# Performance work log

Measured on AMD Instinct MI355X. Metric: run time of the kernel, lower is better.

The kernel has to match this reference:

```python
import jax, jax.numpy as jnp
import numpy as np

D_MODEL = 1024
N_HEADS = 16
HEAD_DIM = D_MODEL // N_HEADS  # 64
BASE = 10000.0
MAX_X, MAX_Y, MAX_Z = 32, 32, 8
NEG_INF = -1e9  # stand-in for float('-inf') in masked_fill; identical after softmax


def _split_dims(head_dim):
    n_pairs = head_dim // 2
    px = n_pairs // 3
    py = n_pairs // 3
    pz = n_pairs - px - py
    return px * 2, py * 2, pz * 2


def _cos_sin_table(dim, max_pos):
    # matches RotaryEmbedding3D._register_cache
    inv_freq = 1.0 / (BASE ** (np.arange(0, dim, 2, dtype=np.float32) / dim))
    t = np.arange(max_pos, dtype=np.float32)[:, None] * inv_freq  # [max_pos, dim/2]
    cos = np.repeat(np.cos(t), 2, axis=-1)  # repeat_interleave(2)
    sin = np.repeat(np.sin(t), 2, axis=-1)
    return jnp.asarray(cos), jnp.asarray(sin)


def _rotate_half(x):
    x1 = x[..., ::2]
    x2 = x[..., 1::2]
    return jnp.stack((-x2, x1), axis=-1).reshape(x.shape)


def setup_inputs() -> dict:
    key = jax.random.key(0)
    k1, k2, k3, k4, k5, k6 = jax.random.split(key, 6)
    B, S = 2, 2048
    hidden_states = jax.random.normal(k1, (B, S, D_MODEL), dtype=jnp.float32)
    w_qkv = jax.random.normal(k2, (D_MODEL, 3 * D_MODEL), dtype=jnp.float32) * 0.02
    w_out = jax.random.normal(k3, (D_MODEL, D_MODEL), dtype=jnp.float32) * 0.02
    px = jax.random.randint(k4, (B, S, 1), 0, MAX_X)
    py = jax.random.randint(k5, (B, S, 1), 0, MAX_Y)
    pz = jax.random.randint(k6, (B, S, 1), 0, MAX_Z)
    pos_xyz = jnp.concatenate([px, py, pz], axis=-1).astype(jnp.int64)
    causal_mask = jnp.triu(jnp.ones((S, S), dtype=bool), k=1)[None, None]  # [1,1,S,S]
    return {"hidden_states": hidden_states, "w_qkv": w_qkv, "w_out": w_out,
            "pos_xyz": pos_xyz, "causal_mask": causal_mask}


def reference(hidden_states, w_qkv, w_out, pos_xyz, causal_mask):
    B, S, D = hidden_states.shape
    H, Hd = N_HEADS, HEAD_DIM
    # fused QKV projection
    qkv = hidden_states @ w_qkv  # [B,S,3D]
    qkv = qkv.reshape(B, S, 3, H, Hd).transpose(2, 0, 3, 1, 4)  # [3,B,H,S,Hd]
    q, k, v = qkv[0], qkv[1], qkv[2]
    # 3D RoPE tables and lookups
    dx, dy, dz = _split_dims(Hd)
    cx, sx = _cos_sin_table(dx, MAX_X)
    cy, sy = _cos_sin_table(dy, MAX_Y)
    cz, sz = _cos_sin_table(dz, MAX_Z)
    ix = jnp.clip(pos_xyz[..., 0], 0, MAX_X - 1)
    iy = jnp.clip(pos_xyz[..., 1], 0, MAX_Y - 1)
    iz = jnp.clip(pos_xyz[..., 2], 0, MAX_Z - 1)
    cos = jnp.concatenate([cx[ix], cy[iy], cz[iz]], axis=-1)[:, None]  # [B,1,S,Hd]
    sin = jnp.concatenate([sx[ix], sy[iy], sz[iz]], axis=-1)[:, None]
    q = q * cos + _rotate_half(q) * sin
    k = k * cos + _rotate_half(k) * sin
    # SDPA with causal bias
    scale = Hd ** -0.5
    scores = jnp.einsum('bhqd,bhkd->bhqk', q, k) * scale
    scores = jnp.where(causal_mask, jnp.asarray(NEG_INF, scores.dtype), scores)
    probs = jax.nn.softmax(scores, axis=-1)
    attn = jnp.einsum('bhqk,bhkd->bhqd', probs, v)
    attn = attn.transpose(0, 2, 1, 3).reshape(B, S, D)
    return attn @ w_out
```

## Files before the change

### kernel.cpp

```cpp
#include <hip/hip_runtime.h>
#include <hip/hip_bf16.h>
#include <math.h>

typedef __bf16 bf16;
typedef __bf16 bf16x8 __attribute__((ext_vector_type(8)));
typedef float f32x4 __attribute__((ext_vector_type(4)));

#define SEQ 2048
#define NHEADS 16
#define HDIM 64
#define DM 1024
#define QKVW 3072
#define NEGBIG -1.0e30f

__device__ __forceinline__ void gload_lds16(const void* g, void* l) {
  __builtin_amdgcn_global_load_lds(
      (const __attribute__((address_space(1))) unsigned int*)g,
      (__attribute__((address_space(3))) unsigned int*)l, 16, 0, 0);
}

template <int CTRL>
__device__ __forceinline__ float dppmovf(float x) {
  return __builtin_bit_cast(
      float, __builtin_amdgcn_mov_dpp(__builtin_bit_cast(int, x), CTRL, 0xf,
                                      0xf, true));
}
__device__ __forceinline__ float rowsum16(float x) {
  x += dppmovf<0xB1>(x);
  x += dppmovf<0x4E>(x);
  x += dppmovf<0x124>(x);
  x += dppmovf<0x128>(x);
  return x;
}

__global__ __launch_bounds__(256) void cvt_f32_bf16(
    const float* __restrict__ in, bf16* __restrict__ out) {
  int i = (blockIdx.x * 256 + threadIdx.x) * 8;
  float4 a = *(const float4*)(in + i);
  float4 b = *(const float4*)(in + i + 4);
  bf16x8 o;
  o[0] = (bf16)a.x; o[1] = (bf16)a.y; o[2] = (bf16)a.z; o[3] = (bf16)a.w;
  o[4] = (bf16)b.x; o[5] = (bf16)b.y; o[6] = (bf16)b.z; o[7] = (bf16)b.w;
  *(bf16x8*)(out + i) = o;
}

__global__ __launch_bounds__(256) void transpose_f32_bf16(
    const float* __restrict__ in, bf16* __restrict__ out, int R, int C) {
  __shared__ float tile[64][65];
  int t = threadIdx.x;
  int c0 = blockIdx.x * 64, r0 = blockIdx.y * 64;
  int col = t & 63, rb = (t >> 6) * 16;
#pragma unroll
  for (int i = 0; i < 16; ++i)
    tile[rb + i][col] = in[(size_t)(r0 + rb + i) * C + c0 + col];
  __syncthreads();
#pragma unroll
  for (int i = 0; i < 16; ++i)
    out[(size_t)(c0 + rb + i) * R + r0 + col] = (bf16)tile[col][rb + i];
}

__global__ __launch_bounds__(256) void rope_tbl_build(
    const int* __restrict__ pos, float2* __restrict__ tbl) {
  const float LN1E4 = 9.210340371976184f;
  int gi = blockIdx.x * 256 + threadIdx.x;
  int m = gi >> 5, pr = gi & 31;
  int axis, d, iloc;
  if (pr < 10)      { axis = 0; d = 20; iloc = pr; }
  else if (pr < 20) { axis = 1; d = 20; iloc = pr - 10; }
  else              { axis = 2; d = 24; iloc = pr - 20; }
  int p = pos[m * 3 + axis];
  int pmax = (axis == 2) ? 7 : 31;
  p = p < 0 ? 0 : (p > pmax ? pmax : p);
  float invf = __expf(-((float)(2 * iloc) / (float)d) * LN1E4);
  float sn, cs;
  __sincosf((float)p * invf, &sn, &cs);
  tbl[gi] = make_float2(cs, sn);
}

__global__ __launch_bounds__(256) void rope_apply(
    bf16* __restrict__ qkv, const float2* __restrict__ tbl) {
  int gi = blockIdx.x * 256 + threadIdx.x;
  int m = gi >> 7, seg = gi & 127;
  bf16* p = qkv + (size_t)m * QKVW + seg * 16;
  bf16x8 a = *(const bf16x8*)p;
  bf16x8 b2 = *(const bf16x8*)(p + 8);
  const float2* t = tbl + m * 32 + (((seg * 16) & 63) >> 1);
#pragma unroll
  for (int j = 0; j < 4; ++j) {
    float2 cs = t[j];
    float e = (float)a[2 * j], o = (float)a[2 * j + 1];
    a[2 * j]     = (bf16)(e * cs.x - o * cs.y);
    a[2 * j + 1] = (bf16)(o * cs.x + e * cs.y);
  }
#pragma unroll
  for (int j = 0; j < 4; ++j) {
    float2 cs = t[4 + j];
    float e = (float)b2[2 * j], o = (float)b2[2 * j + 1];
    b2[2 * j]     = (bf16)(e * cs.x - o * cs.y);
    b2[2 * j + 1] = (bf16)(o * cs.x + e * cs.y);
  }
  *(bf16x8*)p = a;
  *(bf16x8*)(p + 8) = b2;
}

__global__ __launch_bounds__(256) void vT_build(
    const bf16* __restrict__ qkv, bf16* __restrict__ vT) {
  __shared__ bf16 tile[64][65];
  int t = threadIdx.x;
  int s0 = blockIdx.x * 64, bh = blockIdx.y;
  int b = bh >> 4, h = bh & 15;
  const bf16* src = qkv + (size_t)(b * SEQ + s0) * QKVW + 2 * DM + h * 64;
  int col = t & 63, rb = (t >> 6) * 16;
#pragma unroll
  for (int i = 0; i < 16; ++i)
    tile[rb + i][col] = src[(size_t)(rb + i) * QKVW + col];
  __syncthreads();
  bf16* dst = vT + (size_t)bh * HDIM * SEQ + s0;
#pragma unroll
  for (int i = 0; i < 16; ++i)
    dst[(size_t)(rb + i) * SEQ + col] = tile[col][rb + i];
}

template <int OUTBF>
__global__ __launch_bounds__(256) void gemm_bt(
    const bf16* __restrict__ A, const bf16* __restrict__ Bt, void* Cv,
    int M, int N, int K) {
  __shared__ __align__(16) bf16 a_lds[128 * 32];
  __shared__ __align__(16) bf16 b_lds[128 * 32];
  int tid = threadIdx.x;
  int wave = tid >> 6, lane = tid & 63;
  int quad = lane >> 4, l15 = lane & 15;
  int wm = wave >> 1, wn = wave & 1;

  int flat = blockIdx.y * gridDim.x + blockIdx.x;
  int mband = gridDim.y >> 3;
  int xcd = flat & 7, sidx = flat >> 3;
  int m0 = (xcd * mband + (sidx % mband)) * 128;
  int n0 = (sidx / mband) * 128;

  f32x4 acc[4][4] = {};

  for (int kt = 0; kt < K; kt += 32) {
    __syncthreads();
#pragma unroll
    for (int call = 0; call < 2; ++call) {
      int chunk = call * 256 + tid;
      int row = chunk >> 2, cc = (chunk & 3) * 8;
      gload_lds16(A + (size_t)(m0 + row) * K + kt + cc,
                  (char*)a_lds + call * 4096 + wave * 1024);
      gload_lds16(Bt + (size_t)(n0 + row) * K + kt + cc,
                  (char*)b_lds + call * 4096 + wave * 1024);
    }
    __syncthreads();
    bf16x8 af[4], bfr[4];
#pragma unroll
    for (int i = 0; i < 4; ++i) {
      af[i]  = *(const bf16x8*)(a_lds + (wm * 64 + i * 16 + l15) * 32 + quad * 8);
      bfr[i] = *(const bf16x8*)(b_lds + (wn * 64 + i * 16 + l15) * 32 + quad * 8);
    }
#pragma unroll
    for (int mi = 0; mi < 4; ++mi)
#pragma unroll
      for (int ni = 0; ni < 4; ++ni)
        acc[mi][ni] = __builtin_amdgcn_mfma_f32_16x16x32_bf16(
            af[mi], bfr[ni], acc[mi][ni], 0, 0, 0);
  }

#pragma unroll
  for (int mi = 0; mi < 4; ++mi) {
    int mb = m0 + wm * 64 + mi * 16 + quad * 4;
#pragma unroll
    for (int ni = 0; ni < 4; ++ni) {
      int n = n0 + wn * 64 + ni * 16 + l15;
#pragma unroll
      for (int r = 0; r < 4; ++r) {
        if (OUTBF)
          ((bf16*)Cv)[(size_t)(mb + r) * N + n] = (bf16)acc[mi][ni][r];
        else
          ((float*)Cv)[(size_t)(mb + r) * N + n] = acc[mi][ni][r];
      }
    }
  }
}

__global__ __launch_bounds__(256) void attn_fwd(
    const bf16* __restrict__ QKV, const bf16* __restrict__ VT,
    bf16* __restrict__ O) {
  __shared__ __align__(16) bf16 k_lds[64 * 72];
  __shared__ __align__(16) bf16 v_lds[64 * 72];
  __shared__ __align__(16) bf16 p_lds[4][32 * 80];
  const float C2 = 0.18033688011112042f;
  const float C3 = -5.770780163555854f;
  int tid = threadIdx.x;
  int wave = tid >> 6, lane = tid & 63;
  int quad = lane >> 4, l15 = lane & 15;
  int idx = blockIdx.x;
  int bh = idx & 31;
  int g = idx >> 5;
  int qt2 = (g < 8) ? (15 - g) : (g - 8);
  int q0 = qt2 * 128;
  int b = bh >> 4, h = bh & 15;
  const bf16* Qb = QKV + (size_t)b * SEQ * QKVW + h * 64;
  const bf16* Kb = Qb + DM;
  const bf16* VTb = VT + (size_t)bh * HDIM * SEQ;
  bf16* pw = p_lds[wave];

  bf16x8 qf[2][2];
#pragma unroll
  for (int s = 0; s < 2; ++s) {
    const bf16* qr = Qb + (size_t)(q0 + wave * 32 + s * 16 + l15) * QKVW;
    qf[s][0] = *(const bf16x8*)(qr + quad * 8);
    qf[s][1] = *(const bf16x8*)(qr + 32 + quad * 8);
  }

  int r0c = tid >> 3, off0 = (tid & 7) * 8;
  int r1c = r0c + 32;

  int niter = 2 * qt2 + 2;
  f32x4 o_acc[2][4] = {};
  float lsum[2][4] = {};
  int qrow[2][4];
#pragma unroll
  for (int s = 0; s < 2; ++s)
#pragma unroll
    for (int r = 0; r < 4; ++r)
      qrow[s][r] = q0 + wave * 32 + s * 16 + quad * 4 + r;

  bf16x8 kpre0, kpre1, vpre0, vpre1;
  kpre0 = *(const bf16x8*)(Kb + (size_t)r0c * QKVW + off0);
  kpre1 = *(const bf16x8*)(Kb + (size_t)r1c * QKVW + off0);
  vpre0 = *(const bf16x8*)(VTb + (size_t)r0c * SEQ + off0);
  vpre1 = *(const bf16x8*)(VTb + (size_t)r1c * SEQ + off0);

  for (int tkv = 0; tkv < niter; ++tkv) {
    int kv0 = tkv * 64;
    __syncthreads();
    *(bf16x8*)(k_lds + r0c * 72 + off0) = kpre0;
    *(bf16x8*)(k_lds + r1c * 72 + off0) = kpre1;
    *(bf16x8*)(v_lds + r0c * 72 + off0) = vpre0;
    *(bf16x8*)(v_lds + r1c * 72 + off0) = vpre1;
    __syncthreads();
    if (tkv + 1 < niter) {
      int kn = kv0 + 64;
      kpre0 = *(const bf16x8*)(Kb + (size_t)(kn + r0c) * QKVW + off0);
      kpre1 = *(const bf16x8*)(Kb + (size_t)(kn + r1c) * QKVW + off0);
      vpre0 = *(const bf16x8*)(VTb + (size_t)r0c * SEQ + kn + off0);
      vpre1 = *(const bf16x8*)(VTb + (size_t)r1c * SEQ + kn + off0);
    }
    f32x4 s_acc[2][4];
#pragma unroll
    for (int nt = 0; nt < 4; ++nt) {
      const bf16* kr = k_lds + (nt * 16 + l15) * 72;
      bf16x8 kf0 = *(const bf16x8*)(kr + quad * 8);
      bf16x8 kf1 = *(const bf16x8*)(kr + 32 + quad * 8);
#pragma unroll
      for (int s = 0; s < 2; ++s) {
        f32x4 z = {};
        z = __builtin_amdgcn_mfma_f32_16x16x32_bf16(qf[s][0], kf0, z, 0, 0, 0);
        z = __builtin_amdgcn_mfma_f32_16x16x32_bf16(qf[s][1], kf1, z, 0, 0, 0);
        s_acc[s][nt] = z;
      }
    }
    bool diag = (tkv >= 2 * qt2);
#pragma unroll
    for (int s = 0; s < 2; ++s)
#pragma unroll
      for (int r = 0; r < 4; ++r) {
#pragma unroll
        for (int nt = 0; nt < 4; ++nt) {
          float p = __builtin_amdgcn_exp2f(s_acc[s][nt][r] * C2 + C3);
          if (diag && (kv0 + nt * 16 + l15 > qrow[s][r])) p = 0.f;
          lsum[s][r] += p;
          pw[(s * 16 + quad * 4 + r) * 80 + nt * 16 + l15] = (bf16)p;
        }
      }
    __asm__ volatile("s_waitcnt lgkmcnt(0)" ::: "memory");
    bf16x8 vf[4][2];
#pragma unroll
    for (int nt = 0; nt < 4; ++nt) {
      const bf16* vr = v_lds + (nt * 16 + l15) * 72;
      vf[nt][0] = *(const bf16x8*)(vr + quad * 8);
      vf[nt][1] = *(const bf16x8*)(vr + 32 + quad * 8);
    }
#pragma unroll
    for (int s = 0; s < 2; ++s) {
      bf16x8 pf0 = *(const bf16x8*)(pw + (s * 16 + l15) * 80 + quad * 8);
      bf16x8 pf1 = *(const bf16x8*)(pw + (s * 16 + l15) * 80 + 32 + quad * 8);
#pragma unroll
      for (int nt = 0; nt < 4; ++nt) {
        o_acc[s][nt] = __builtin_amdgcn_mfma_f32_16x16x32_bf16(
            pf0, vf[nt][0], o_acc[s][nt], 0, 0, 0);
        o_acc[s][nt] = __builtin_amdgcn_mfma_f32_16x16x32_bf16(
            pf1, vf[nt][1], o_acc[s][nt], 0, 0, 0);
      }
    }
  }
#pragma unroll
  for (int s = 0; s < 2; ++s)
#pragma unroll
    for (int r = 0; r < 4; ++r) {
      float inv = 1.f / rowsum16(lsum[s][r]);
      int sq = qrow[s][r];
#pragma unroll
      for (int nt = 0; nt < 4; ++nt)
        O[((size_t)(b * SEQ + sq)) * DM + h * HDIM + nt * 16 + l15] =
            (bf16)(o_acc[s][nt][r] * inv);
    }
}

extern "C" void kernel_launch(void* const* d_in, const int* in_sizes, int n_in,
                              void* d_out, int out_size, void* d_ws,
                              size_t ws_size, hipStream_t stream) {
  const float* hidden = (const float*)d_in[0];
  const float* w_qkv  = (const float*)d_in[1];
  const float* w_out  = (const float*)d_in[2];
  const int*   pos    = (const int*)d_in[3];
  float* out = (float*)d_out;

  char* ws = (char*)d_ws;
  bf16* wqkvT  = (bf16*)ws;  ws += (size_t)3072 * 1024 * 2;
  bf16* woutT  = (bf16*)ws;  ws += (size_t)1024 * 1024 * 2;
  bf16* hid_bf = (bf16*)ws;  ws += (size_t)4096 * 1024 * 2;
  bf16* qkv_ws = (bf16*)ws;  ws += (size_t)4096 * 3072 * 2;
  bf16* vT_ws  = (bf16*)ws;  ws += (size_t)32 * SEQ * HDIM * 2;
  float2* ropetbl = (float2*)ws;
  bf16* attn_ws = hid_bf;

  cvt_f32_bf16<<<dim3(2048), 256, 0, stream>>>(hidden, hid_bf);
  transpose_f32_bf16<<<dim3(48, 16), 256, 0, stream>>>(w_qkv, wqkvT, 1024, 3072);
  transpose_f32_bf16<<<dim3(16, 16), 256, 0, stream>>>(w_out, woutT, 1024, 1024);
  rope_tbl_build<<<dim3(512), 256, 0, stream>>>(pos, ropetbl);
  gemm_bt<1><<<dim3(24, 32), 256, 0, stream>>>(
      hid_bf, wqkvT, qkv_ws, 4096, 3072, 1024);
  rope_apply<<<dim3(2048), 256, 0, stream>>>(qkv_ws, ropetbl);
  vT_build<<<dim3(32, 32), 256, 0, stream>>>(qkv_ws, vT_ws);
  attn_fwd<<<dim3(512), 256, 0, stream>>>(qkv_ws, vT_ws, attn_ws);
  gemm_bt<0><<<dim3(8, 32), 256, 0, stream>>>(
      attn_ws, woutT, out, 4096, 1024, 1024);
}
```

Before: 220.8 us.

## Merge prep and post-QKV kernels and halve attention query tile to 64 rows

The fp32→bf16 conversion, both weight transposes and the RoPE table build now run as one block-indexed prep launch. RoPE application and the V transpose now share one post_qkv launch, which cuts the number of kernel launches and the gaps between them. The attention kernel now processes 64 query rows per block (one 16-row slice per wave) instead of 128, doubling the grid to 1024 blocks for better CU occupancy and load balance. The trade-off is that each K/V tile is reused by half as many query rows, so K/V traffic per query roughly doubles.

```diff
diff --git a/kernel.cpp b/kernel.cpp
--- a/kernel.cpp
+++ b/kernel.cpp
@@ -11,7 +11,6 @@
 #define HDIM 64
 #define DM 1024
 #define QKVW 3072
-#define NEGBIG -1.0e30f
 
 __device__ __forceinline__ void gload_lds16(const void* g, void* l) {
   __builtin_amdgcn_global_load_lds(
@@ -33,92 +32,96 @@
   return x;
 }
 
-__global__ __launch_bounds__(256) void cvt_f32_bf16(
-    const float* __restrict__ in, bf16* __restrict__ out) {
-  int i = (blockIdx.x * 256 + threadIdx.x) * 8;
-  float4 a = *(const float4*)(in + i);
-  float4 b = *(const float4*)(in + i + 4);
-  bf16x8 o;
-  o[0] = (bf16)a.x; o[1] = (bf16)a.y; o[2] = (bf16)a.z; o[3] = (bf16)a.w;
-  o[4] = (bf16)b.x; o[5] = (bf16)b.y; o[6] = (bf16)b.z; o[7] = (bf16)b.w;
-  *(bf16x8*)(out + i) = o;
-}
-
-__global__ __launch_bounds__(256) void transpose_f32_bf16(
-    const float* __restrict__ in, bf16* __restrict__ out, int R, int C) {
+__global__ __launch_bounds__(256) void prep(
+    const float* __restrict__ hidden, const float* __restrict__ w_qkv,
+    const float* __restrict__ w_out, const int* __restrict__ pos,
+    bf16* __restrict__ hid_bf, bf16* __restrict__ wqkvT,
+    bf16* __restrict__ woutT, float2* __restrict__ tbl) {
   __shared__ float tile[64][65];
-  int t = threadIdx.x;
-  int c0 = blockIdx.x * 64, r0 = blockIdx.y * 64;
-  int col = t & 63, rb = (t >> 6) * 16;
-#pragma unroll
-  for (int i = 0; i < 16; ++i)
-    tile[rb + i][col] = in[(size_t)(r0 + rb + i) * C + c0 + col];
-  __syncthreads();
-#pragma unroll
-  for (int i = 0; i < 16; ++i)
-    out[(size_t)(c0 + rb + i) * R + r0 + col] = (bf16)tile[col][rb + i];
-}
-
-__global__ __launch_bounds__(256) void rope_tbl_build(
-    const int* __restrict__ pos, float2* __restrict__ tbl) {
-  const float LN1E4 = 9.210340371976184f;
-  int gi = blockIdx.x * 256 + threadIdx.x;
-  int m = gi >> 5, pr = gi & 31;
-  int axis, d, iloc;
-  if (pr < 10)      { axis = 0; d = 20; iloc = pr; }
-  else if (pr < 20) { axis = 1; d = 20; iloc = pr - 10; }
-  else              { axis = 2; d = 24; iloc = pr - 20; }
-  int p = pos[m * 3 + axis];
-  int pmax = (axis == 2) ? 7 : 31;
-  p = p < 0 ? 0 : (p > pmax ? pmax : p);
-  float invf = __expf(-((float)(2 * iloc) / (float)d) * LN1E4);
-  float sn, cs;
-  __sincosf((float)p * invf, &sn, &cs);
-  tbl[gi] = make_float2(cs, sn);
-}
-
-__global__ __launch_bounds__(256) void rope_apply(
-    bf16* __restrict__ qkv, const float2* __restrict__ tbl) {
-  int gi = blockIdx.x * 256 + threadIdx.x;
-  int m = gi >> 7, seg = gi & 127;
-  bf16* p = qkv + (size_t)m * QKVW + seg * 16;
-  bf16x8 a = *(const bf16x8*)p;
-  bf16x8 b2 = *(const bf16x8*)(p + 8);
-  const float2* t = tbl + m * 32 + (((seg * 16) & 63) >> 1);
-#pragma unroll
-  for (int j = 0; j < 4; ++j) {
-    float2 cs = t[j];
-    float e = (float)a[2 * j], o = (float)a[2 * j + 1];
-    a[2 * j]     = (bf16)(e * cs.x - o * cs.y);
-    a[2 * j + 1] = (bf16)(o * cs.x + e * cs.y);
-  }
-#pragma unroll
-  for (int j = 0; j < 4; ++j) {
-    float2 cs = t[4 + j];
-    float e = (float)b2[2 * j], o = (float)b2[2 * j + 1];
-    b2[2 * j]     = (bf16)(e * cs.x - o * cs.y);
-    b2[2 * j + 1] = (bf16)(o * cs.x + e * cs.y);
-  }
-  *(bf16x8*)p = a;
-  *(bf16x8*)(p + 8) = b2;
-}
-
-__global__ __launch_bounds__(256) void vT_build(
-    const bf16* __restrict__ qkv, bf16* __restrict__ vT) {
-  __shared__ bf16 tile[64][65];
-  int t = threadIdx.x;
-  int s0 = blockIdx.x * 64, bh = blockIdx.y;
-  int b = bh >> 4, h = bh & 15;
-  const bf16* src = qkv + (size_t)(b * SEQ + s0) * QKVW + 2 * DM + h * 64;
-  int col = t & 63, rb = (t >> 6) * 16;
-#pragma unroll
-  for (int i = 0; i < 16; ++i)
-    tile[rb + i][col] = src[(size_t)(rb + i) * QKVW + col];
-  __syncthreads();
-  bf16* dst = vT + (size_t)bh * HDIM * SEQ + s0;
-#pragma unroll
-  for (int i = 0; i < 16; ++i)
-    dst[(size_t)(rb + i) * SEQ + col] = tile[col][rb + i];
+  int idx = blockIdx.x, tid = threadIdx.x;
+  if (idx < 2048) {
+    int i = (idx * 256 + tid) * 8;
+    float4 a = *(const float4*)(hidden + i);
+    float4 b = *(const float4*)(hidden + i + 4);
+    bf16x8 o;
+    o[0] = (bf16)a.x; o[1] = (bf16)a.y; o[2] = (bf16)a.z; o[3] = (bf16)a.w;
+    o[4] = (bf16)b.x; o[5] = (bf16)b.y; o[6] = (bf16)b.z; o[7] = (bf16)b.w;
+    *(bf16x8*)(hid_bf + i) = o;
+  } else if (idx < 3072) {
+    const float* in; bf16* out; int R, C, t;
+    if (idx < 2816) { t = idx - 2048; in = w_qkv; out = wqkvT; R = 1024; C = 3072; }
+    else            { t = idx - 2816; in = w_out; out = woutT; R = 1024; C = 1024; }
+    int nbx = C >> 6;
+    int c0 = (t % nbx) * 64, r0 = (t / nbx) * 64;
+    int col = tid & 63, rb = (tid >> 6) * 16;
+#pragma unroll
+    for (int i = 0; i < 16; ++i)
+      tile[rb + i][col] = in[(size_t)(r0 + rb + i) * C + c0 + col];
+    __syncthreads();
+#pragma unroll
+    for (int i = 0; i < 16; ++i)
+      out[(size_t)(c0 + rb + i) * R + r0 + col] = (bf16)tile[col][rb + i];
+  } else {
+    const float LN1E4 = 9.210340371976184f;
+    int gi = (idx - 3072) * 256 + tid;
+    int m = gi >> 5, pr = gi & 31;
+    int axis, d, iloc;
+    if (pr < 10)      { axis = 0; d = 20; iloc = pr; }
+    else if (pr < 20) { axis = 1; d = 20; iloc = pr - 10; }
+    else              { axis = 2; d = 24; iloc = pr - 20; }
+    int p = pos[m * 3 + axis];
+    int pmax = (axis == 2) ? 7 : 31;
+    p = p < 0 ? 0 : (p > pmax ? pmax : p);
+    float invf = __expf(-((float)(2 * iloc) / (float)d) * LN1E4);
+    float sn, cs;
+    __sincosf((float)p * invf, &sn, &cs);
+    tbl[gi] = make_float2(cs, sn);
+  }
+}
+
+__global__ __launch_bounds__(256) void post_qkv(
+    bf16* __restrict__ qkv, const float2* __restrict__ tbl,
+    bf16* __restrict__ vT) {
+  __shared__ bf16 btile[64][65];
+  int idx = blockIdx.x, tid = threadIdx.x;
+  if (idx < 2048) {
+    int gi = idx * 256 + tid;
+    int m = gi >> 7, seg = gi & 127;
+    bf16* p = qkv + (size_t)m * QKVW + seg * 16;
+    bf16x8 a = *(const bf16x8*)p;
+    bf16x8 b2 = *(const bf16x8*)(p + 8);
+    const float2* t = tbl + m * 32 + (((seg * 16) & 63) >> 1);
+#pragma unroll
+    for (int j = 0; j < 4; ++j) {
+      float2 cs = t[j];
+      float e = (float)a[2 * j], o = (float)a[2 * j + 1];
+      a[2 * j]     = (bf16)(e * cs.x - o * cs.y);
+      a[2 * j + 1] = (bf16)(o * cs.x + e * cs.y);
+    }
+#pragma unroll
+    for (int j = 0; j < 4; ++j) {
+      float2 cs = t[4 + j];
+      float e = (float)b2[2 * j], o = (float)b2[2 * j + 1];
+      b2[2 * j]     = (bf16)(e * cs.x - o * cs.y);
+      b2[2 * j + 1] = (bf16)(o * cs.x + e * cs.y);
+    }
+    *(bf16x8*)p = a;
+    *(bf16x8*)(p + 8) = b2;
+  } else {
+    int t = idx - 2048;
+    int s0 = (t & 31) * 64, bh = t >> 5;
+    int b = bh >> 4, h = bh & 15;
+    const bf16* src = qkv + (size_t)(b * SEQ + s0) * QKVW + 2 * DM + h * 64;
+    int col = tid & 63, rb = (tid >> 6) * 16;
+#pragma unroll
+    for (int i = 0; i < 16; ++i)
+      btile[rb + i][col] = src[(size_t)(rb + i) * QKVW + col];
+    __syncthreads();
+    bf16* dst = vT + (size_t)bh * HDIM * SEQ + s0;
+#pragma unroll
+    for (int i = 0; i < 16; ++i)
+      dst[(size_t)(rb + i) * SEQ + col] = btile[col][rb + i];
+  }
 }
 
 template <int OUTBF>
@@ -188,7 +191,7 @@
     bf16* __restrict__ O) {
   __shared__ __align__(16) bf16 k_lds[64 * 72];
   __shared__ __align__(16) bf16 v_lds[64 * 72];
-  __shared__ __align__(16) bf16 p_lds[4][32 * 80];
+  __shared__ __align__(16) bf16 p_lds[4][16 * 80];
   const float C2 = 0.18033688011112042f;
   const float C3 = -5.770780163555854f;
   int tid = threadIdx.x;
@@ -197,34 +200,27 @@
   int idx = blockIdx.x;
   int bh = idx & 31;
   int g = idx >> 5;
-  int qt2 = (g < 8) ? (15 - g) : (g - 8);
-  int q0 = qt2 * 128;
+  int qt = (g < 16) ? (31 - g) : (g - 16);
+  int q0 = qt * 64;
   int b = bh >> 4, h = bh & 15;
   const bf16* Qb = QKV + (size_t)b * SEQ * QKVW + h * 64;
   const bf16* Kb = Qb + DM;
   const bf16* VTb = VT + (size_t)bh * HDIM * SEQ;
   bf16* pw = p_lds[wave];
 
-  bf16x8 qf[2][2];
-#pragma unroll
-  for (int s = 0; s < 2; ++s) {
-    const bf16* qr = Qb + (size_t)(q0 + wave * 32 + s * 16 + l15) * QKVW;
-    qf[s][0] = *(const bf16x8*)(qr + quad * 8);
-    qf[s][1] = *(const bf16x8*)(qr + 32 + quad * 8);
-  }
+  const bf16* qr = Qb + (size_t)(q0 + wave * 16 + l15) * QKVW;
+  bf16x8 qf0 = *(const bf16x8*)(qr + quad * 8);
+  bf16x8 qf1 = *(const bf16x8*)(qr + 32 + quad * 8);
 
   int r0c = tid >> 3, off0 = (tid & 7) * 8;
   int r1c = r0c + 32;
 
-  int niter = 2 * qt2 + 2;
-  f32x4 o_acc[2][4] = {};
-  float lsum[2][4] = {};
-  int qrow[2][4];
-#pragma unroll
-  for (int s = 0; s < 2; ++s)
-#pragma unroll
-    for (int r = 0; r < 4; ++r)
-      qrow[s][r] = q0 + wave * 32 + s * 16 + quad * 4 + r;
+  int niter = qt + 1;
+  f32x4 o_acc[4] = {};
+  float lsum[4] = {};
+  int qrow[4];
+#pragma unroll
+  for (int r = 0; r < 4; ++r) qrow[r] = q0 + wave * 16 + quad * 4 + r;
 
   bf16x8 kpre0, kpre1, vpre0, vpre1;
   kpre0 = *(const bf16x8*)(Kb + (size_t)r0c * QKVW + off0);
@@ -247,65 +243,49 @@
       vpre0 = *(const bf16x8*)(VTb + (size_t)r0c * SEQ + kn + off0);
       vpre1 = *(const bf16x8*)(VTb + (size_t)r1c * SEQ + kn + off0);
     }
-    f32x4 s_acc[2][4];
+    f32x4 s_acc[4];
 #pragma unroll
     for (int nt = 0; nt < 4; ++nt) {
       const bf16* kr = k_lds + (nt * 16 + l15) * 72;
       bf16x8 kf0 = *(const bf16x8*)(kr + quad * 8);
       bf16x8 kf1 = *(const bf16x8*)(kr + 32 + quad * 8);
-#pragma unroll
-      for (int s = 0; s < 2; ++s) {
-        f32x4 z = {};
-        z = __builtin_amdgcn_mfma_f32_16x16x32_bf16(qf[s][0], kf0, z, 0, 0, 0);
-        z = __builtin_amdgcn_mfma_f32_16x16x32_bf16(qf[s][1], kf1, z, 0, 0, 0);
-        s_acc[s][nt] = z;
+      f32x4 z = {};
+      z = __builtin_amdgcn_mfma_f32_16x16x32_bf16(qf0, kf0, z, 0, 0, 0);
+      z = __builtin_amdgcn_mfma_f32_16x16x32_bf16(qf1, kf1, z, 0, 0, 0);
+      s_acc[nt] = z;
+    }
+    bool diag = (tkv == qt);
+#pragma unroll
+    for (int r = 0; r < 4; ++r) {
+#pragma unroll
+      for (int nt = 0; nt < 4; ++nt) {
+        float p = __builtin_amdgcn_exp2f(s_acc[nt][r] * C2 + C3);
+        if (diag && (kv0 + nt * 16 + l15 > qrow[r])) p = 0.f;
+        lsum[r] += p;
+        pw[(quad * 4 + r) * 80 + nt * 16 + l15] = (bf16)p;
       }
     }
-    bool diag = (tkv >= 2 * qt2);
-#pragma unroll
-    for (int s = 0; s < 2; ++s)
-#pragma unroll
-      for (int r = 0; r < 4; ++r) {
-#pragma unroll
-        for (int nt = 0; nt < 4; ++nt) {
-          float p = __builtin_amdgcn_exp2f(s_acc[s][nt][r] * C2 + C3);
-          if (diag && (kv0 + nt * 16 + l15 > qrow[s][r])) p = 0.f;
-          lsum[s][r] += p;
-          pw[(s * 16 + quad * 4 + r) * 80 + nt * 16 + l15] = (bf16)p;
-        }
-      }
     __asm__ volatile("s_waitcnt lgkmcnt(0)" ::: "memory");
-    bf16x8 vf[4][2];
+    bf16x8 pf0 = *(const bf16x8*)(pw + l15 * 80 + quad * 8);
+    bf16x8 pf1 = *(const bf16x8*)(pw + l15 * 80 + 32 + quad * 8);
 #pragma unroll
     for (int nt = 0; nt < 4; ++nt) {
       const bf16* vr = v_lds + (nt * 16 + l15) * 72;
-      vf[nt][0] = *(const bf16x8*)(vr + quad * 8);
-      vf[nt][1] = *(const bf16x8*)(vr + 32 + quad * 8);
-    }
-#pragma unroll
-    for (int s = 0; s < 2; ++s) {
-      bf16x8 pf0 = *(const bf16x8*)(pw + (s * 16 + l15) * 80 + quad * 8);
-      bf16x8 pf1 = *(const bf16x8*)(pw + (s * 16 + l15) * 80 + 32 + quad * 8);
-#pragma unroll
-      for (int nt = 0; nt < 4; ++nt) {
-        o_acc[s][nt] = __builtin_amdgcn_mfma_f32_16x16x32_bf16(
-            pf0, vf[nt][0], o_acc[s][nt], 0, 0, 0);
-        o_acc[s][nt] = __builtin_amdgcn_mfma_f32_16x16x32_bf16(
-            pf1, vf[nt][1], o_acc[s][nt], 0, 0, 0);
-      }
-    }
-  }
-#pragma unroll
-  for (int s = 0; s < 2; ++s)
-#pragma unroll
-    for (int r = 0; r < 4; ++r) {
-      float inv = 1.f / rowsum16(lsum[s][r]);
-      int sq = qrow[s][r];
-#pragma unroll
-      for (int nt = 0; nt < 4; ++nt)
-        O[((size_t)(b * SEQ + sq)) * DM + h * HDIM + nt * 16 + l15] =
-            (bf16)(o_acc[s][nt][r] * inv);
-    }
+      bf16x8 vf0 = *(const bf16x8*)(vr + quad * 8);
+      bf16x8 vf1 = *(const bf16x8*)(vr + 32 + quad * 8);
+      o_acc[nt] = __builtin_amdgcn_mfma_f32_16x16x32_bf16(pf0, vf0, o_acc[nt], 0, 0, 0);
+      o_acc[nt] = __builtin_amdgcn_mfma_f32_16x16x32_bf16(pf1, vf1, o_acc[nt], 0, 0, 0);
+    }
+  }
+#pragma unroll
+  for (int r = 0; r < 4; ++r) {
+    float inv = 1.f / rowsum16(lsum[r]);
+    int sq = qrow[r];
+#pragma unroll
+    for (int nt = 0; nt < 4; ++nt)
+      O[((size_t)(b * SEQ + sq)) * DM + h * HDIM + nt * 16 + l15] =
+          (bf16)(o_acc[nt][r] * inv);
+  }
 }
 
 extern "C" void kernel_launch(void* const* d_in, const int* in_sizes, int n_in,
@@ -326,15 +306,12 @@
   float2* ropetbl = (float2*)ws;
   bf16* attn_ws = hid_bf;
 
-  cvt_f32_bf16<<<dim3(2048), 256, 0, stream>>>(hidden, hid_bf);
-  transpose_f32_bf16<<<dim3(48, 16), 256, 0, stream>>>(w_qkv, wqkvT, 1024, 3072);
-  transpose_f32_bf16<<<dim3(16, 16), 256, 0, stream>>>(w_out, woutT, 1024, 1024);
-  rope_tbl_build<<<dim3(512), 256, 0, stream>>>(pos, ropetbl);
+  prep<<<dim3(3584), 256, 0, stream>>>(hidden, w_qkv, w_out, pos,
+                                       hid_bf, wqkvT, woutT, ropetbl);
   gemm_bt<1><<<dim3(24, 32), 256, 0, stream>>>(
       hid_bf, wqkvT, qkv_ws, 4096, 3072, 1024);
-  rope_apply<<<dim3(2048), 256, 0, stream>>>(qkv_ws, ropetbl);
-  vT_build<<<dim3(32, 32), 256, 0, stream>>>(qkv_ws, vT_ws);
-  attn_fwd<<<dim3(512), 256, 0, stream>>>(qkv_ws, vT_ws, attn_ws);
+  post_qkv<<<dim3(3072), 256, 0, stream>>>(qkv_ws, ropetbl, vT_ws);
+  attn_fwd<<<dim3(1024), 256, 0, stream>>>(qkv_ws, vT_ws, attn_ws);
   gemm_bt<0><<<dim3(8, 32), 256, 0, stream>>>(
       attn_ws, woutT, out, 4096, 1024, 1024);
 }
```

Measured after the change: 205.6 us. -6.9%, faster.
